# Kernel tuning notes

Measured on AMD Instinct MI355X. Metric: run time of the kernel, lower is better.

## Reference

```python
import jax, jax.numpy as jnp
import numpy as np

EPS = 1e-7  # keras backend epsilon

def setup_inputs() -> dict:
    key = jax.random.key(0)
    k1, k2, k3, k4, k5 = jax.random.split(key, 5)
    B, S, D, A = 64, 2048, 512, 256
    x = jax.random.normal(k1, (B, S, D), dtype=jnp.float32)
    mask = jax.random.randint(k2, (B, S), 0, 2) > 0
    # keras 'normal' initializer: RandomNormal(stddev=0.05)
    W = 0.05 * jax.random.normal(k3, (D, A), dtype=jnp.float32)
    b = 0.05 * jax.random.normal(k4, (A,), dtype=jnp.float32)
    u = 0.05 * jax.random.normal(k5, (A, 1), dtype=jnp.float32)
    return {"x": x, "mask": mask, "W": W, "b": b, "u": u}

def reference(x, mask, W, b, u):
    # x: [B,S,D], W: [D,A], b: [A], u: [A,1]
    uit = jnp.tanh(jnp.einsum('bsd,da->bsa', x, W) + b)   # [B,S,A]
    ait = jnp.einsum('bsa,a->bs', uit, u[:, 0])           # [B,S]
    ait = jnp.exp(ait)
    ait = ait * mask.astype(x.dtype)
    ait = ait / (jnp.sum(ait, axis=1, keepdims=True) + EPS)  # [B,S]
    return jnp.einsum('bsd,bs->bd', x, ait)               # [B,D]
```

## Files before the change

### kernel.cpp

```cpp
#include <hip/hip_runtime.h>
#include <stdint.h>

#define B_ 64
#define S_ 2048
#define D_ 512
#define A_ 256
#define TM 64
#define NTILES 32
#define EPS 1e-7f

typedef short bf16x8 __attribute__((ext_vector_type(8)));
typedef float f32x4  __attribute__((ext_vector_type(4)));

#define WS_WT   0
#define WS_PART 262144
#define WS_Z    4456448
#define WS_FLAG 4456704

__device__ __forceinline__ uint32_t f32pair_to_bf16(float a, float b) {
  uint32_t ua = __float_as_uint(a), ub = __float_as_uint(b);
  ua = (ua + 0x7fffu + ((ua >> 16) & 1u)) >> 16;
  ub = (ub + 0x7fffu + ((ub >> 16) & 1u)) & 0xffff0000u;
  return ua | ub;
}

__global__ __launch_bounds__(256) void prep_kernel(
    const float* __restrict__ W, const void* __restrict__ mask,
    uint16_t* __restrict__ Wt, float* __restrict__ Z, int* __restrict__ flag)
{
  int i = blockIdx.x * 256 + threadIdx.x;
  if (i < A_ * D_) {
    int a = i >> 9;
    int d = i & (D_ - 1);
    uint32_t u = __float_as_uint(W[d * A_ + a]);
    u = (u + 0x7fffu + ((u >> 16) & 1u)) >> 16;
    Wt[i] = (uint16_t)u;
  } else if (i < A_ * D_ + B_) {
    Z[i - A_ * D_] = 0.0f;
  }
  if (blockIdx.x == 0 && threadIdx.x < 64) {
    const uint32_t* mw = (const uint32_t*)mask;
    int hit = 0;
    for (int k = 0; k < 16; ++k) {
      uint32_t v = mw[threadIdx.x + 64 * k];
      uint32_t b0 = v & 0xff, b1 = (v >> 8) & 0xff, b2 = (v >> 16) & 0xff, b3 = v >> 24;
      if (b0 <= 1u && b1 <= 1u && b2 <= 1u && b3 <= 1u && (b1 | b2 | b3)) hit = 1;
    }
    hit = __any(hit);
    if (threadIdx.x == 0) *flag = hit ? 1 : 0;
  }
}

__global__ __launch_bounds__(256, 2) void att_main(
    const float* __restrict__ x, const void* __restrict__ mask,
    const float* __restrict__ bias, const float* __restrict__ uvec,
    const uint16_t* __restrict__ Wt, float* __restrict__ part,
    float* __restrict__ Z, const int* __restrict__ flag)
{
  __shared__ uint16_t xs[TM * D_];
  __shared__ float sp[4][TM];
  __shared__ float ev[TM];

  const int tid  = threadIdx.x;
  const int bx   = blockIdx.x;
  const int b    = bx >> 5;
  const int tile = bx & 31;
  const int s0   = tile * TM;

  const float* xb = x + ((size_t)b * S_ + (size_t)s0) * D_;
  #pragma unroll
  for (int c = 0; c < 16; ++c) {
    int p   = c * 256 + tid;
    int row = p >> 6;
    int ch  = p & 63;
    const float* src = xb + row * D_ + ch * 8;
    float4 v0 = *(const float4*)(src);
    float4 v1 = *(const float4*)(src + 4);
    uint4 pk;
    pk.x = f32pair_to_bf16(v0.x, v0.y);
    pk.y = f32pair_to_bf16(v0.z, v0.w);
    pk.z = f32pair_to_bf16(v1.x, v1.y);
    pk.w = f32pair_to_bf16(v1.z, v1.w);
    int cc = ch ^ (row & 7);
    *(uint4*)(&xs[row * D_ + cc * 8]) = pk;
  }
  __syncthreads();

  const int l  = tid & 63;
  const int w  = tid >> 6;
  const int lr = l & 15;
  const int lg = l >> 4;

  f32x4 acc[4][4];
  #pragma unroll
  for (int mt = 0; mt < 4; ++mt)
    #pragma unroll
    for (int nt = 0; nt < 4; ++nt)
      acc[mt][nt] = (f32x4){0.f, 0.f, 0.f, 0.f};

  const uint16_t* WtBase = Wt + (size_t)(w * 64 + lr) * D_;

  #pragma unroll 4
  for (int ks = 0; ks < 16; ++ks) {
    bf16x8 af[4], bfr[4];
    #pragma unroll
    for (int mt = 0; mt < 4; ++mt) {
      int row = mt * 16 + lr;
      int cc  = (ks * 4 + lg) ^ (lr & 7);
      af[mt]  = *(const bf16x8*)(&xs[row * D_ + cc * 8]);
    }
    #pragma unroll
    for (int nt = 0; nt < 4; ++nt)
      bfr[nt] = *(const bf16x8*)(WtBase + nt * 16 * D_ + ks * 32 + lg * 8);
    #pragma unroll
    for (int mt = 0; mt < 4; ++mt)
      #pragma unroll
      for (int nt = 0; nt < 4; ++nt)
        acc[mt][nt] = __builtin_amdgcn_mfma_f32_16x16x32_bf16(af[mt], bfr[nt], acc[mt][nt], 0, 0, 0);
  }

  float bn[4], un[4];
  #pragma unroll
  for (int nt = 0; nt < 4; ++nt) {
    int n = w * 64 + nt * 16 + lr;
    bn[nt] = bias[n];
    un[nt] = uvec[n];
  }
  #pragma unroll
  for (int mt = 0; mt < 4; ++mt) {
    #pragma unroll
    for (int r = 0; r < 4; ++r) {
      float ssum = 0.0f;
      #pragma unroll
      for (int nt = 0; nt < 4; ++nt) {
        float v  = acc[mt][nt][r] + bn[nt];
        float av = fabsf(v);
        float e2 = __expf(-2.0f * av);
        float t  = (1.0f - e2) / (1.0f + e2);
        ssum += copysignf(t, v) * un[nt];
      }
      ssum += __shfl_xor(ssum, 1);
      ssum += __shfl_xor(ssum, 2);
      ssum += __shfl_xor(ssum, 4);
      ssum += __shfl_xor(ssum, 8);
      if (lr == 0) sp[w][mt * 16 + lg * 4 + r] = ssum;
    }
  }
  __syncthreads();

  if (tid < TM) {
    float score = sp[0][tid] + sp[1][tid] + sp[2][tid] + sp[3][tid];
    int midx = b * S_ + s0 + tid;
    int mval;
    if (*flag) mval = ((const unsigned char*)mask)[midx] != 0;
    else       mval = ((const int*)mask)[midx] != 0;
    float e = mval ? __expf(score) : 0.0f;
    ev[tid] = e;
    float tot = e;
    #pragma unroll
    for (int o = 1; o < 64; o <<= 1) tot += __shfl_xor(tot, o);
    if (tid == 0) atomicAdd(&Z[b], tot);
  }
  __syncthreads();

  {
    int d0 = tid * 2;
    int c0 = d0 >> 3;
    int j  = d0 & 7;
    float a0 = 0.0f, a1 = 0.0f;
    for (int s = 0; s < TM; ++s) {
      int cc = c0 ^ (s & 7);
      uint32_t v = *(const uint32_t*)(&xs[s * D_ + cc * 8 + j]);
      float e = ev[s];
      a0 = fmaf(e, __uint_as_float(v << 16), a0);
      a1 = fmaf(e, __uint_as_float(v & 0xffff0000u), a1);
    }
    float2 st; st.x = a0; st.y = a1;
    *(float2*)(&part[(size_t)bx * D_ + d0]) = st;
  }
}

__global__ __launch_bounds__(256) void scale_kernel(
    const float* __restrict__ part, const float* __restrict__ Z,
    float* __restrict__ out)
{
  int idx = blockIdx.x * 256 + threadIdx.x;
  int b = idx >> 9;
  int d = idx & (D_ - 1);
  float s = 0.0f;
  #pragma unroll 8
  for (int t = 0; t < NTILES; ++t)
    s += part[(size_t)(b * NTILES + t) * D_ + d];
  out[idx] = s / (Z[b] + EPS);
}

extern "C" void kernel_launch(void* const* d_in, const int* in_sizes, int n_in,
                              void* d_out, int out_size, void* d_ws, size_t ws_size,
                              hipStream_t stream)
{
  const float* x    = (const float*)d_in[0];
  const void*  mask = d_in[1];
  const float* W    = (const float*)d_in[2];
  const float* bias = (const float*)d_in[3];
  const float* u    = (const float*)d_in[4];
  float* out = (float*)d_out;

  char* ws = (char*)d_ws;
  uint16_t* Wt  = (uint16_t*)(ws + WS_WT);
  float* part   = (float*)(ws + WS_PART);
  float* Z      = (float*)(ws + WS_Z);
  int*   flag   = (int*)(ws + WS_FLAG);

  int prep_threads = A_ * D_ + B_;
  prep_kernel<<<(prep_threads + 255) / 256, 256, 0, stream>>>(W, mask, Wt, Z, flag);
  att_main<<<B_ * NTILES, 256, 0, stream>>>(x, mask, bias, u, Wt, part, Z, flag);
  scale_kernel<<<(B_ * D_ + 255) / 256, 256, 0, stream>>>(part, Z, out);
}
```

Measured before the change: 435.1 us.

## Halve sequence tile, raise occupancy, and reduce partial sums via atomics

Shrinks each block's sequence tile from 64 to 32 rows, doubling the grid and raising launch bounds to 4 blocks per CU so more waves are resident. Per-tile partial sums are now atomically accumulated into a zeroed [B,D] numerator instead of stored to a partials buffer, so the scale kernel only divides. The x load is split into two batches of loads followed by conversion to raise memory-level parallelism, and tanh uses a hardware reciprocal instead of a division. Smaller tiles reload W fragments twice as often per row of x, and float atomics add contention plus nondeterministic summation order.

```diff
diff --git a/kernel.cpp b/kernel.cpp
--- a/kernel.cpp
+++ b/kernel.cpp
@@ -5,17 +5,17 @@
 #define S_ 2048
 #define D_ 512
 #define A_ 256
-#define TM 64
-#define NTILES 32
+#define TM 32
+#define NTILES 64
 #define EPS 1e-7f
 
 typedef short bf16x8 __attribute__((ext_vector_type(8)));
 typedef float f32x4  __attribute__((ext_vector_type(4)));
 
 #define WS_WT   0
-#define WS_PART 262144
-#define WS_Z    4456448
-#define WS_FLAG 4456704
+#define WS_NUM  262144
+#define WS_Z    393216
+#define WS_FLAG 393472
 
 __device__ __forceinline__ uint32_t f32pair_to_bf16(float a, float b) {
   uint32_t ua = __float_as_uint(a), ub = __float_as_uint(b);
@@ -26,7 +26,8 @@
 
 __global__ __launch_bounds__(256) void prep_kernel(
     const float* __restrict__ W, const void* __restrict__ mask,
-    uint16_t* __restrict__ Wt, float* __restrict__ Z, int* __restrict__ flag)
+    uint16_t* __restrict__ Wt, float* __restrict__ num,
+    float* __restrict__ Z, int* __restrict__ flag)
 {
   int i = blockIdx.x * 256 + threadIdx.x;
   if (i < A_ * D_) {
@@ -35,8 +36,10 @@
     uint32_t u = __float_as_uint(W[d * A_ + a]);
     u = (u + 0x7fffu + ((u >> 16) & 1u)) >> 16;
     Wt[i] = (uint16_t)u;
-  } else if (i < A_ * D_ + B_) {
-    Z[i - A_ * D_] = 0.0f;
+  } else if (i < A_ * D_ + B_ * D_) {
+    num[i - A_ * D_] = 0.0f;
+  } else if (i < A_ * D_ + B_ * D_ + B_) {
+    Z[i - A_ * D_ - B_ * D_] = 0.0f;
   }
   if (blockIdx.x == 0 && threadIdx.x < 64) {
     const uint32_t* mw = (const uint32_t*)mask;
@@ -51,10 +54,10 @@
   }
 }
 
-__global__ __launch_bounds__(256, 2) void att_main(
+__global__ __launch_bounds__(256, 4) void att_main(
     const float* __restrict__ x, const void* __restrict__ mask,
     const float* __restrict__ bias, const float* __restrict__ uvec,
-    const uint16_t* __restrict__ Wt, float* __restrict__ part,
+    const uint16_t* __restrict__ Wt, float* __restrict__ num,
     float* __restrict__ Z, const int* __restrict__ flag)
 {
   __shared__ uint16_t xs[TM * D_];
@@ -63,26 +66,36 @@
 
   const int tid  = threadIdx.x;
   const int bx   = blockIdx.x;
-  const int b    = bx >> 5;
-  const int tile = bx & 31;
+  const int b    = bx >> 6;
+  const int tile = bx & 63;
   const int s0   = tile * TM;
 
   const float* xb = x + ((size_t)b * S_ + (size_t)s0) * D_;
   #pragma unroll
-  for (int c = 0; c < 16; ++c) {
-    int p   = c * 256 + tid;
-    int row = p >> 6;
-    int ch  = p & 63;
-    const float* src = xb + row * D_ + ch * 8;
-    float4 v0 = *(const float4*)(src);
-    float4 v1 = *(const float4*)(src + 4);
-    uint4 pk;
-    pk.x = f32pair_to_bf16(v0.x, v0.y);
-    pk.y = f32pair_to_bf16(v0.z, v0.w);
-    pk.z = f32pair_to_bf16(v1.x, v1.y);
-    pk.w = f32pair_to_bf16(v1.z, v1.w);
-    int cc = ch ^ (row & 7);
-    *(uint4*)(&xs[row * D_ + cc * 8]) = pk;
+  for (int half = 0; half < 2; ++half) {
+    float4 v[4][2];
+    #pragma unroll
+    for (int c = 0; c < 4; ++c) {
+      int p   = (half * 4 + c) * 256 + tid;
+      int row = p >> 6;
+      int ch  = p & 63;
+      const float* src = xb + row * D_ + ch * 8;
+      v[c][0] = *(const float4*)(src);
+      v[c][1] = *(const float4*)(src + 4);
+    }
+    #pragma unroll
+    for (int c = 0; c < 4; ++c) {
+      int p   = (half * 4 + c) * 256 + tid;
+      int row = p >> 6;
+      int ch  = p & 63;
+      uint4 pk;
+      pk.x = f32pair_to_bf16(v[c][0].x, v[c][0].y);
+      pk.y = f32pair_to_bf16(v[c][0].z, v[c][0].w);
+      pk.z = f32pair_to_bf16(v[c][1].x, v[c][1].y);
+      pk.w = f32pair_to_bf16(v[c][1].z, v[c][1].w);
+      int cc = ch ^ (row & 7);
+      *(uint4*)(&xs[row * D_ + cc * 8]) = pk;
+    }
   }
   __syncthreads();
 
@@ -91,9 +104,9 @@
   const int lr = l & 15;
   const int lg = l >> 4;
 
-  f32x4 acc[4][4];
-  #pragma unroll
-  for (int mt = 0; mt < 4; ++mt)
+  f32x4 acc[2][4];
+  #pragma unroll
+  for (int mt = 0; mt < 2; ++mt)
     #pragma unroll
     for (int nt = 0; nt < 4; ++nt)
       acc[mt][nt] = (f32x4){0.f, 0.f, 0.f, 0.f};
@@ -102,9 +115,9 @@
 
   #pragma unroll 4
   for (int ks = 0; ks < 16; ++ks) {
-    bf16x8 af[4], bfr[4];
-    #pragma unroll
-    for (int mt = 0; mt < 4; ++mt) {
+    bf16x8 af[2], bfr[4];
+    #pragma unroll
+    for (int mt = 0; mt < 2; ++mt) {
       int row = mt * 16 + lr;
       int cc  = (ks * 4 + lg) ^ (lr & 7);
       af[mt]  = *(const bf16x8*)(&xs[row * D_ + cc * 8]);
@@ -113,7 +126,7 @@
     for (int nt = 0; nt < 4; ++nt)
       bfr[nt] = *(const bf16x8*)(WtBase + nt * 16 * D_ + ks * 32 + lg * 8);
     #pragma unroll
-    for (int mt = 0; mt < 4; ++mt)
+    for (int mt = 0; mt < 2; ++mt)
       #pragma unroll
       for (int nt = 0; nt < 4; ++nt)
         acc[mt][nt] = __builtin_amdgcn_mfma_f32_16x16x32_bf16(af[mt], bfr[nt], acc[mt][nt], 0, 0, 0);
@@ -127,7 +140,7 @@
     un[nt] = uvec[n];
   }
   #pragma unroll
-  for (int mt = 0; mt < 4; ++mt) {
+  for (int mt = 0; mt < 2; ++mt) {
     #pragma unroll
     for (int r = 0; r < 4; ++r) {
       float ssum = 0.0f;
@@ -136,7 +149,7 @@
         float v  = acc[mt][nt][r] + bn[nt];
         float av = fabsf(v);
         float e2 = __expf(-2.0f * av);
-        float t  = (1.0f - e2) / (1.0f + e2);
+        float t  = 1.0f - 2.0f * e2 * __builtin_amdgcn_rcpf(1.0f + e2);
         ssum += copysignf(t, v) * un[nt];
       }
       ssum += __shfl_xor(ssum, 1);
@@ -158,7 +171,7 @@
     ev[tid] = e;
     float tot = e;
     #pragma unroll
-    for (int o = 1; o < 64; o <<= 1) tot += __shfl_xor(tot, o);
+    for (int o = 1; o < TM; o <<= 1) tot += __shfl_xor(tot, o);
     if (tid == 0) atomicAdd(&Z[b], tot);
   }
   __syncthreads();
@@ -168,6 +181,7 @@
     int c0 = d0 >> 3;
     int j  = d0 & 7;
     float a0 = 0.0f, a1 = 0.0f;
+    #pragma unroll 8
     for (int s = 0; s < TM; ++s) {
       int cc = c0 ^ (s & 7);
       uint32_t v = *(const uint32_t*)(&xs[s * D_ + cc * 8 + j]);
@@ -175,23 +189,18 @@
       a0 = fmaf(e, __uint_as_float(v << 16), a0);
       a1 = fmaf(e, __uint_as_float(v & 0xffff0000u), a1);
     }
-    float2 st; st.x = a0; st.y = a1;
-    *(float2*)(&part[(size_t)bx * D_ + d0]) = st;
+    atomicAdd(&num[b * D_ + d0], a0);
+    atomicAdd(&num[b * D_ + d0 + 1], a1);
   }
 }
 
 __global__ __launch_bounds__(256) void scale_kernel(
-    const float* __restrict__ part, const float* __restrict__ Z,
+    const float* __restrict__ num, const float* __restrict__ Z,
     float* __restrict__ out)
 {
   int idx = blockIdx.x * 256 + threadIdx.x;
   int b = idx >> 9;
-  int d = idx & (D_ - 1);
-  float s = 0.0f;
-  #pragma unroll 8
-  for (int t = 0; t < NTILES; ++t)
-    s += part[(size_t)(b * NTILES + t) * D_ + d];
-  out[idx] = s / (Z[b] + EPS);
+  out[idx] = num[idx] / (Z[b] + EPS);
 }
 
 extern "C" void kernel_launch(void* const* d_in, const int* in_sizes, int n_in,
@@ -207,12 +216,12 @@
 
   char* ws = (char*)d_ws;
   uint16_t* Wt  = (uint16_t*)(ws + WS_WT);
-  float* part   = (float*)(ws + WS_PART);
+  float* num    = (float*)(ws + WS_NUM);
   float* Z      = (float*)(ws + WS_Z);
   int*   flag   = (int*)(ws + WS_FLAG);
 
-  int prep_threads = A_ * D_ + B_;
-  prep_kernel<<<(prep_threads + 255) / 256, 256, 0, stream>>>(W, mask, Wt, Z, flag);
-  att_main<<<B_ * NTILES, 256, 0, stream>>>(x, mask, bias, u, Wt, part, Z, flag);
-  scale_kernel<<<(B_ * D_ + 255) / 256, 256, 0, stream>>>(part, Z, out);
-}
+  int prep_threads = A_ * D_ + B_ * D_ + B_;
+  prep_kernel<<<(prep_threads + 255) / 256, 256, 0, stream>>>(W, mask, Wt, num, Z, flag);
+  att_main<<<B_ * NTILES, 256, 0, stream>>>(x, mask, bias, u, Wt, num, Z, flag);
+  scale_kernel<<<(B_ * D_ + 255) / 256, 256, 0, stream>>>(num, Z, out);
+}
```

After: 445.2 us. 2.3% more time.
